# Kernel tuning notes

Measured on AMD Instinct MI355X. Metric: run time of the kernel, lower is better.

Reference implementation:

```python
import jax, jax.numpy as jnp
import numpy as np

N_NODES = 20000
N_EDGES = 320000
F_IN, H1, H2, N_CLS = 128, 512, 256, 40
NEG_SLOPE = 0.2


def _glorot(key, shape):
    lim = float(np.sqrt(6.0 / (shape[0] + shape[-1])))
    return jax.random.uniform(key, shape, jnp.float32, -lim, lim)


def setup_inputs() -> dict:
    key = jax.random.key(0)
    ks = jax.random.split(key, 12)
    x = jax.random.normal(ks[0], (N_NODES, F_IN), jnp.float32)
    edge_index = jax.random.randint(ks[1], (2, N_EDGES), 0, N_NODES, jnp.int64)
    params = {}
    dims = [(F_IN, H1), (H1, H2), (H2, N_CLS)]
    for i, (din, dout) in enumerate(dims, start=1):
        params[f"W{i}"] = _glorot(ks[3 * i - 1], (din, dout))
        params[f"a{i}s"] = _glorot(ks[3 * i], (1, dout))[0]
        params[f"a{i}d"] = _glorot(ks[3 * i + 1], (1, dout))[0]
        params[f"b{i}"] = jnp.zeros((dout,), jnp.float32)
    return {"x": x, "edge_index": edge_index, **params}


def gat_conv(x, src, dst, W, a_src, a_dst, b, num_nodes):
    # PyG GATConv, heads=1: h = xW; e_ij = LeakyReLU(a_src.h_j + a_dst.h_i)
    # alpha = softmax over incoming edges of target i; out_i = sum_j alpha_ij h_j + b
    h = x @ W                                        # [N, Dout]
    alpha_s = h @ a_src                              # [N]
    alpha_d = h @ a_dst                              # [N]
    e = jax.nn.leaky_relu(alpha_s[src] + alpha_d[dst], NEG_SLOPE)  # [E]
    m = jax.ops.segment_max(e, dst, num_segments=num_nodes)        # [N]
    ex = jnp.exp(e - m[dst])
    denom = jax.ops.segment_sum(ex, dst, num_segments=num_nodes)   # [N]
    alpha = ex / denom[dst]
    out = jax.ops.segment_sum(alpha[:, None] * h[src], dst, num_segments=num_nodes)
    return out + b


def reference(x, edge_index, W1, a1s, a1d, b1, W2, a2s, a2d, b2, W3, a3s, a3d, b3):
    n = x.shape[0]
    # PyG GATConv adds self-loops by default
    loops = jnp.arange(n, dtype=edge_index.dtype)
    src = jnp.concatenate([edge_index[0], loops])
    dst = jnp.concatenate([edge_index[1], loops])
    h = jax.nn.relu(gat_conv(x, src, dst, W1, a1s, a1d, b1, n))
    h = jax.nn.relu(gat_conv(h, src, dst, W2, a2s, a2d, b2, n))
    h = gat_conv(h, src, dst, W3, a3s, a3d, b3, n)
    return jax.nn.log_softmax(h, axis=1)
```

## Files before the change

### kernel.cpp

```cpp
#include <hip/hip_runtime.h>
#include <math.h>

#define N_NODES 20000
#define N_EDGESC 320000
#define ET (N_EDGESC + N_NODES)
#define F_IN 128
#define H1 512
#define H2 256
#define N_CLS 40
#define NEG_SLOPE 0.2f

typedef __attribute__((ext_vector_type(8))) short short8;
typedef __attribute__((ext_vector_type(4))) float floatx4;

__device__ __forceinline__ unsigned short f2bf(float x) {
    unsigned u = __float_as_uint(x);
    unsigned r = (u + 0x7fffu + ((u >> 16) & 1u)) >> 16;
    return (unsigned short)r;
}
__device__ __forceinline__ float bflo(unsigned v) { return __uint_as_float(v << 16); }
__device__ __forceinline__ float bfhi(unsigned v) { return __uint_as_float(v & 0xffff0000u); }
__device__ __forceinline__ float leaky(float e) { return (e > 0.f) ? e : e * NEG_SLOPE; }

template <int DIN, bool IN_BF16>
__device__ __forceinline__ void gemv2_body(int node, int lane, const void* __restrict__ in,
                                           const float* __restrict__ wvs,
                                           const float* __restrict__ wvd,
                                           float* __restrict__ als, float* __restrict__ ald) {
    constexpr int C = DIN / 64;
    float ss = 0.f, sd = 0.f;
    if constexpr (IN_BF16) {
        const unsigned short* r = (const unsigned short*)in + (size_t)node * DIN + lane * C;
        float f[C];
        if constexpr (C == 8) {
            uint4 v = *(const uint4*)r;
            f[0] = bflo(v.x); f[1] = bfhi(v.x); f[2] = bflo(v.y); f[3] = bfhi(v.y);
            f[4] = bflo(v.z); f[5] = bfhi(v.z); f[6] = bflo(v.w); f[7] = bfhi(v.w);
        } else {
            uint2 v = *(const uint2*)r;
            f[0] = bflo(v.x); f[1] = bfhi(v.x); f[2] = bflo(v.y); f[3] = bfhi(v.y);
        }
        #pragma unroll
        for (int c = 0; c < C; ++c) {
            ss += f[c] * wvs[lane * C + c];
            sd += f[c] * wvd[lane * C + c];
        }
    } else {
        const float* r = (const float*)in + (size_t)node * DIN + lane * 2;
        float2 v = *(const float2*)r;
        ss = v.x * wvs[lane * 2] + v.y * wvs[lane * 2 + 1];
        sd = v.x * wvd[lane * 2] + v.y * wvd[lane * 2 + 1];
    }
    #pragma unroll
    for (int off = 32; off; off >>= 1) {
        ss += __shfl_xor(ss, off);
        sd += __shfl_xor(sd, off);
    }
    if (lane == 0) { als[node] = ss; ald[node] = sd; }
}

#define NCT (F_IN * H1 + H1 * H2 + H2 * N_CLS)
#define PB_CASTX 2500
#define PB_CASTT ((NCT + 255) / 256)
#define PB_WA 224
#define PB_ZERO ((N_NODES + 255) / 256)

__global__ __launch_bounds__(256) void prep_kernel(
        const float* __restrict__ x, unsigned short* __restrict__ xb,
        const float* __restrict__ W1, unsigned short* __restrict__ w1t,
        const float* __restrict__ a1s, const float* __restrict__ a1d,
        const float* __restrict__ W2, unsigned short* __restrict__ w2t,
        const float* __restrict__ a2s, const float* __restrict__ a2d,
        const float* __restrict__ W3, unsigned short* __restrict__ w3t,
        const float* __restrict__ a3s, const float* __restrict__ a3d,
        float* __restrict__ wab, int* __restrict__ deg) {
    int bid = blockIdx.x, t = threadIdx.x;
    if (bid < PB_CASTX) {
        int i = (bid * 256 + t) * 4;
        float4 v = *(const float4*)(x + i);
        ushort4 o = { f2bf(v.x), f2bf(v.y), f2bf(v.z), f2bf(v.w) };
        *(ushort4*)(xb + i) = o;
    } else if (bid < PB_CASTX + PB_CASTT) {
        int i = (bid - PB_CASTX) * 256 + t;
        if (i < F_IN * H1) {
            int k = i >> 9, n = i & 511;
            w1t[n * F_IN + k] = f2bf(W1[i]);
        } else if (i < F_IN * H1 + H1 * H2) {
            int j = i - F_IN * H1;
            int k = j >> 8, n = j & 255;
            w2t[n * H1 + k] = f2bf(W2[j]);
        } else if (i < NCT) {
            int j = i - (F_IN * H1 + H1 * H2);
            int k = j / N_CLS, n = j - k * N_CLS;
            w3t[n * H2 + k] = f2bf(W3[j]);
        }
    } else if (bid < PB_CASTX + PB_CASTT + PB_WA) {
        int lane = t & 63;
        int row = (bid - PB_CASTX - PB_CASTT) * 4 + (t >> 6);
        const float *W, *vs, *vd;
        float *os, *od;
        int N, k;
        if (row < 128)      { k = row;       W = W1; vs = a1s; vd = a1d; os = wab;        od = wab + 128;  N = H1; }
        else if (row < 640) { k = row - 128; W = W2; vs = a2s; vd = a2d; os = wab + 256;  od = wab + 768;  N = H2; }
        else                { k = row - 640; W = W3; vs = a3s; vd = a3d; os = wab + 1280; od = wab + 1536; N = N_CLS; }
        const float* r = W + (size_t)k * N;
        float ss = 0.f, sd = 0.f;
        for (int n = lane; n < N; n += 64) {
            float v = r[n];
            ss += v * vs[n];
            sd += v * vd[n];
        }
        #pragma unroll
        for (int off = 32; off; off >>= 1) {
            ss += __shfl_xor(ss, off);
            sd += __shfl_xor(sd, off);
        }
        if (lane == 0) { os[k] = ss; od[k] = sd; }
    } else {
        int i = (bid - PB_CASTX - PB_CASTT - PB_WA) * 256 + t;
        if (i < N_NODES) deg[i] = 0;
    }
}

#define CB_CNT ((ET + 255) / 256)

__global__ __launch_bounds__(256) void count_gemv1_kernel(
        const int* __restrict__ ei, int* __restrict__ deg,
        const float* __restrict__ x, const float* __restrict__ wab,
        float* __restrict__ als1, float* __restrict__ ald1) {
    int bid = blockIdx.x, t = threadIdx.x;
    if (bid < CB_CNT) {
        int e = bid * 256 + t;
        if (e < ET) {
            int d = (e < N_EDGESC) ? ei[N_EDGESC + e] : (e - N_EDGESC);
            atomicAdd(&deg[d], 1);
        }
    } else {
        int node = (bid - CB_CNT) * 4 + (t >> 6);
        if (node < N_NODES)
            gemv2_body<F_IN, false>(node, t & 63, x, wab, wab + 128, als1, ald1);
    }
}

__global__ __launch_bounds__(1024) void scan_kernel(const int* __restrict__ deg,
                                                    int* __restrict__ rowptr,
                                                    int* __restrict__ writeptr) {
    __shared__ int sums[1024];
    int t = threadIdx.x;
    const int per = (N_NODES + 1023) / 1024;
    int base = t * per;
    int local = 0;
    for (int i = 0; i < per; ++i) {
        int idx = base + i;
        if (idx < N_NODES) local += deg[idx];
    }
    sums[t] = local;
    __syncthreads();
    for (int off = 1; off < 1024; off <<= 1) {
        int add = (t >= off) ? sums[t - off] : 0;
        __syncthreads();
        sums[t] += add;
        __syncthreads();
    }
    int run = sums[t] - local;
    for (int i = 0; i < per; ++i) {
        int idx = base + i;
        if (idx < N_NODES) {
            rowptr[idx] = run;
            writeptr[idx] = run;
            run += deg[idx];
        }
    }
    if (t == 1023) rowptr[N_NODES] = sums[1023];
}

__global__ void fill_kernel(const int* __restrict__ ei, int* __restrict__ writeptr,
                            int* __restrict__ csr_src) {
    int e = blockIdx.x * blockDim.x + threadIdx.x;
    if (e >= ET) return;
    int s, d;
    if (e < N_EDGESC) { s = ei[e]; d = ei[N_EDGESC + e]; }
    else { s = d = e - N_EDGESC; }
    int pos = atomicAdd(&writeptr[d], 1);
    csr_src[pos] = s;
}

#define LDT 40
#define LSO 66

template <int MT, int NT, bool BIASRELU, bool OUT_BF16, int GDIN, bool GBF16>
__global__ __launch_bounds__(256) void gemm_fused(
        const unsigned short* __restrict__ A, const unsigned short* __restrict__ Bt,
        void* __restrict__ Cp, const float* __restrict__ bias,
        int M, int K, int N, int gemm_blocks,
        const void* __restrict__ gin, const float* __restrict__ wvs,
        const float* __restrict__ wvd, float* __restrict__ als, float* __restrict__ ald) {
    constexpr int MI = MT / 64;
    __shared__ unsigned short As[MT * LDT];
    __shared__ unsigned short Bs[64 * LDT];
    __shared__ unsigned short Ls[64 * LSO];
    int bid = blockIdx.x, t = threadIdx.x;
    int w = t >> 6, lane = t & 63;

    if (bid >= gemm_blocks) {
        if constexpr (GDIN > 0) {
            int node = (bid - gemm_blocks) * 4 + w;
            if (node < N_NODES)
                gemv2_body<GDIN, GBF16>(node, lane, gin, wvs, wvd, als, ald);
        }
        return;
    }

    int quad = lane >> 4, l16 = lane & 15;
    int bm = (bid / NT) * MT, bn = (bid % NT) * 64;

    int ar0 = t >> 2;
    int ak = (t & 3) * 8;

    floatx4 acc[MI][4];
    #pragma unroll
    for (int i = 0; i < MI; ++i)
        #pragma unroll
        for (int j = 0; j < 4; ++j) acc[i][j] = (floatx4){0.f, 0.f, 0.f, 0.f};

    uint4 pa0 = {0,0,0,0}, pa1 = {0,0,0,0}, pb = {0,0,0,0};
    {
        int gm0 = bm + ar0, gn = bn + ar0;
        if (gm0 < M) pa0 = *(const uint4*)(A + (size_t)gm0 * K + ak);
        if constexpr (MI == 2) {
            int gm1 = bm + 64 + ar0;
            if (gm1 < M) pa1 = *(const uint4*)(A + (size_t)gm1 * K + ak);
        }
        if (gn < N) pb = *(const uint4*)(Bt + (size_t)gn * K + ak);
    }

    for (int k0 = 0; k0 < K; k0 += 32) {
        *(uint4*)(&As[ar0 * LDT + ak]) = pa0;
        if constexpr (MI == 2) *(uint4*)(&As[(64 + ar0) * LDT + ak]) = pa1;
        *(uint4*)(&Bs[ar0 * LDT + ak]) = pb;
        __syncthreads();

        int kn = k0 + 32;
        if (kn < K) {
            int gm0 = bm + ar0, gn = bn + ar0;
            pa0 = (gm0 < M) ? *(const uint4*)(A + (size_t)gm0 * K + kn + ak) : (uint4){0,0,0,0};
            if constexpr (MI == 2) {
                int gm1 = bm + 64 + ar0;
                pa1 = (gm1 < M) ? *(const uint4*)(A + (size_t)gm1 * K + kn + ak) : (uint4){0,0,0,0};
            }
            pb = (gn < N) ? *(const uint4*)(Bt + (size_t)gn * K + kn + ak) : (uint4){0,0,0,0};
        }

        short8 a[MI], b[4];
        #pragma unroll
        for (int mi = 0; mi < MI; ++mi)
            a[mi] = *(short8*)(&As[(w * (MT / 4) + mi * 16 + l16) * LDT + quad * 8]);
        #pragma unroll
        for (int ni = 0; ni < 4; ++ni)
            b[ni] = *(short8*)(&Bs[(ni * 16 + l16) * LDT + quad * 8]);
        #pragma unroll
        for (int mi = 0; mi < MI; ++mi)
            #pragma unroll
            for (int ni = 0; ni < 4; ++ni)
                acc[mi][ni] = __builtin_amdgcn_mfma_f32_16x16x32_bf16(a[mi], b[ni], acc[mi][ni], 0, 0, 0);
        __syncthreads();
    }

    if constexpr (OUT_BF16) {
        #pragma unroll
        for (int mi = 0; mi < MI; ++mi) {
            #pragma unroll
            for (int ni = 0; ni < 4; ++ni) {
                int col = bn + ni * 16 + l16;
                #pragma unroll
                for (int r = 0; r < 4; ++r) {
                    float v = acc[mi][ni][r];
                    if constexpr (BIASRELU) v = fmaxf(v + bias[col], 0.f);
                    Ls[(w * 16 + quad * 4 + r) * LSO + ni * 16 + l16] = f2bf(v);
                }
            }
            __syncthreads();
            #pragma unroll
            for (int i = 0; i < 2; ++i) {
                int idx = t + i * 256;
                int lrow = idx >> 3, c8 = (idx & 7) * 8;
                int grow = bm + (lrow >> 4) * (MT / 4) + mi * 16 + (lrow & 15);
                if (grow < M)
                    *(uint4*)((unsigned short*)Cp + (size_t)grow * N + bn + c8) =
                        *(uint4*)(&Ls[lrow * LSO + c8]);
            }
            __syncthreads();
        }
    } else {
        #pragma unroll
        for (int mi = 0; mi < MI; ++mi) {
            #pragma unroll
            for (int r = 0; r < 4; ++r) {
                int row = bm + w * (MT / 4) + mi * 16 + quad * 4 + r;
                if (row >= M) continue;
                #pragma unroll
                for (int ni = 0; ni < 4; ++ni) {
                    int col = bn + ni * 16 + l16;
                    if (col < N) ((float*)Cp)[(size_t)row * N + col] = acc[mi][ni][r];
                }
            }
        }
    }
}

template <int DOUT, bool BIAS, bool RELU, bool LSM, bool IN_BF16, bool OUT_BF16>
__global__ __launch_bounds__(256) void agg_kernel(const void* __restrict__ h,
                                                  const float* __restrict__ as,
                                                  const float* __restrict__ ad,
                                                  const int* __restrict__ rowptr,
                                                  const int* __restrict__ csr_src,
                                                  const float* __restrict__ bias,
                                                  void* __restrict__ outp) {
    constexpr int C = (DOUT + 63) / 64;
    int wave = threadIdx.x >> 6, lane = threadIdx.x & 63;
    int node = blockIdx.x * 4 + wave;
    if (node >= N_NODES) return;
    int beg = rowptr[node], end = rowptr[node + 1];
    float adi = ad[node];

    int k0 = beg + lane;
    bool has0 = k0 < end;
    int sj = has0 ? csr_src[k0] : 0;
    float ej = -INFINITY;
    if (has0) ej = leaky(as[sj] + adi);

    float m = ej;
    for (int k = k0 + 64; k < end; k += 64) m = fmaxf(m, leaky(as[csr_src[k]] + adi));
    #pragma unroll
    for (int off = 32; off; off >>= 1) m = fmaxf(m, __shfl_xor(m, off));

    float den = has0 ? expf(ej - m) : 0.f;
    for (int k = k0 + 64; k < end; k += 64) den += expf(leaky(as[csr_src[k]] + adi) - m);
    #pragma unroll
    for (int off = 32; off; off >>= 1) den += __shfl_xor(den, off);
    float invden = 1.f / den;

    float wgt = has0 ? expf(ej - m) * invden : 0.f;

    float acc[C];
    #pragma unroll
    for (int c = 0; c < C; ++c) acc[c] = 0.f;

    auto fetch = [&](int s, float* f) {
        if constexpr (IN_BF16) {
            const unsigned short* hr = (const unsigned short*)h + (size_t)s * DOUT + lane * C;
            if constexpr (C == 8) {
                uint4 v = *(const uint4*)hr;
                f[0] = bflo(v.x); f[1] = bfhi(v.x); f[2] = bflo(v.y); f[3] = bfhi(v.y);
                f[4] = bflo(v.z); f[5] = bfhi(v.z); f[6] = bflo(v.w); f[7] = bfhi(v.w);
            } else if constexpr (C == 4) {
                uint2 v = *(const uint2*)hr;
                f[0] = bflo(v.x); f[1] = bfhi(v.x); f[2] = bflo(v.y); f[3] = bfhi(v.y);
            } else {
                unsigned v = *(const unsigned*)hr;
                f[0] = bflo(v); f[1] = bfhi(v);
            }
        } else {
            if (lane < DOUT) f[0] = ((const float*)h)[(size_t)s * DOUT + lane];
            else f[0] = 0.f;
        }
    };

    int cnt0 = min(64, end - beg);
    int j = 0;
    for (; j + 7 < cnt0; j += 8) {
        int s[8]; float a[8]; float f[8][C];
        #pragma unroll
        for (int u = 0; u < 8; ++u) { s[u] = __shfl(sj, j + u); a[u] = __shfl(wgt, j + u); }
        #pragma unroll
        for (int u = 0; u < 8; ++u) fetch(s[u], f[u]);
        #pragma unroll
        for (int u = 0; u < 8; ++u)
            #pragma unroll
            for (int c = 0; c < C; ++c) acc[c] += a[u] * f[u][c];
    }
    for (; j < cnt0; ++j) {
        int s0 = __shfl(sj, j);
        float a0 = __shfl(wgt, j);
        float f0[C];
        fetch(s0, f0);
        #pragma unroll
        for (int c = 0; c < C; ++c) acc[c] += a0 * f0[c];
    }
    for (int base = beg + 64; base < end; base += 64) {
        int cnt = min(64, end - base);
        int sx = 0; float wx = 0.f;
        if (lane < cnt) {
            sx = csr_src[base + lane];
            wx = expf(leaky(as[sx] + adi) - m) * invden;
        }
        for (int jj = 0; jj < cnt; ++jj) {
            int s0 = __shfl(sx, jj);
            float a0 = __shfl(wx, jj);
            float f0[C];
            fetch(s0, f0);
            #pragma unroll
            for (int c = 0; c < C; ++c) acc[c] += a0 * f0[c];
        }
    }

    if constexpr (!LSM) {
        #pragma unroll
        for (int c = 0; c < C; ++c) {
            int col = lane * C + c;
            if (DOUT % 64 == 0 || col < DOUT) {
                float v = acc[c];
                if constexpr (BIAS) v += bias[col];
                if constexpr (RELU) v = fmaxf(v, 0.f);
                if constexpr (OUT_BF16)
                    ((unsigned short*)outp)[(size_t)node * DOUT + col] = f2bf(v);
                else
                    ((float*)outp)[(size_t)node * DOUT + col] = v;
            }
        }
    } else {
        float v = (lane < DOUT) ? (acc[0] + bias[lane]) : -INFINITY;
        float mm = v;
        #pragma unroll
        for (int off = 32; off; off >>= 1) mm = fmaxf(mm, __shfl_xor(mm, off));
        float ex = (lane < DOUT) ? expf(v - mm) : 0.f;
        float Z = ex;
        #pragma unroll
        for (int off = 32; off; off >>= 1) Z += __shfl_xor(Z, off);
        if (lane < DOUT) ((float*)outp)[(size_t)node * DOUT + lane] = v - mm - logf(Z);
    }
}


extern "C" void kernel_launch(void* const* d_in, const int* in_sizes, int n_in,
                              void* d_out, int out_size, void* d_ws, size_t ws_size,
                              hipStream_t stream) {
    const float* x   = (const float*)d_in[0];
    const int*   ei  = (const int*)d_in[1];
    const float* W1  = (const float*)d_in[2];
    const float* a1s = (const float*)d_in[3];
    const float* a1d = (const float*)d_in[4];
    const float* b1  = (const float*)d_in[5];
    const float* W2  = (const float*)d_in[6];
    const float* a2s = (const float*)d_in[7];
    const float* a2d = (const float*)d_in[8];
    const float* b2  = (const float*)d_in[9];
    const float* W3  = (const float*)d_in[10];
    const float* a3s = (const float*)d_in[11];
    const float* a3d = (const float*)d_in[12];
    const float* b3  = (const float*)d_in[13];
    float* out = (float*)d_out;

    char* ws = (char*)d_ws;
    size_t off = 0;
    auto alloc = [&](size_t bytes) {
        void* p = ws + off;
        off = (off + bytes + 255) & ~(size_t)255;
        return p;
    };
    int*            deg      = (int*)alloc(N_NODES * 4);
    int*            writeptr = (int*)alloc(N_NODES * 4);
    int*            rowptr   = (int*)alloc((N_NODES + 1) * 4);
    int*            csr_src  = (int*)alloc((size_t)ET * 4);
    float*          alph     = (float*)alloc((size_t)6 * N_NODES * 4);
    float*          wab      = (float*)alloc(1792 * 4);
    unsigned short* xb       = (unsigned short*)alloc((size_t)N_NODES * F_IN * 2);
    unsigned short* w1t      = (unsigned short*)alloc((size_t)H1 * F_IN * 2);
    unsigned short* w2t      = (unsigned short*)alloc((size_t)H2 * H1 * 2);
    unsigned short* w3t      = (unsigned short*)alloc((size_t)N_CLS * H2 * 2);
    unsigned short* zb       = (unsigned short*)alloc((size_t)N_NODES * F_IN * 2);
    unsigned short* y1       = (unsigned short*)alloc((size_t)N_NODES * H1 * 2);
    unsigned short* h2       = (unsigned short*)alloc((size_t)N_NODES * H2 * 2);
    float*          h3       = (float*)alloc((size_t)N_NODES * N_CLS * 4);
    (void)alloc(128 * 1024);

    unsigned short* y2 = y1;

    float* als1 = alph + 0 * N_NODES; float* ald1 = alph + 1 * N_NODES;
    float* als2 = alph + 2 * N_NODES; float* ald2 = alph + 3 * N_NODES;
    float* als3 = alph + 4 * N_NODES; float* ald3 = alph + 5 * N_NODES;

    dim3 blk(256);
    int nodeblocks = (N_NODES + 3) / 4;
    const int mt128 = (N_NODES + 127) / 128;
    const int mt64  = (N_NODES + 63) / 64;

    prep_kernel<<<PB_CASTX + PB_CASTT + PB_WA + PB_ZERO, blk, 0, stream>>>(
        x, xb, W1, w1t, a1s, a1d, W2, w2t, a2s, a2d, W3, w3t, a3s, a3d, wab, deg);
    count_gemv1_kernel<<<CB_CNT + nodeblocks, blk, 0, stream>>>(ei, deg, x, wab, als1, ald1);
    scan_kernel<<<1, 1024, 0, stream>>>(deg, rowptr, writeptr);
    fill_kernel<<<(ET + 255) / 256, blk, 0, stream>>>(ei, writeptr, csr_src);

    agg_kernel<F_IN, false, false, false, true, true><<<nodeblocks, blk, 0, stream>>>(
        xb, als1, ald1, rowptr, csr_src, nullptr, zb);
    gemm_fused<128, 8, true, true, 0, false><<<8 * mt128, blk, 0, stream>>>(
        zb, w1t, y1, b1, N_NODES, F_IN, H1, 8 * mt128,
        nullptr, nullptr, nullptr, nullptr, nullptr);
    gemm_fused<128, 4, false, true, H1, true><<<4 * mt128 + nodeblocks, blk, 0, stream>>>(
        y1, w2t, h2, nullptr, N_NODES, H1, H2, 4 * mt128,
        y1, wab + 256, wab + 768, als2, ald2);
    agg_kernel<H2, true, true, false, true, true><<<nodeblocks, blk, 0, stream>>>(
        h2, als2, ald2, rowptr, csr_src, b2, y2);
    gemm_fused<64, 1, false, false, H2, true><<<mt64 + nodeblocks, blk, 0, stream>>>(
        y2, w3t, h3, nullptr, N_NODES, H2, N_CLS, mt64,
        y2, wab + 1280, wab + 1536, als3, ald3);
    agg_kernel<N_CLS, true, false, true, false, false><<<nodeblocks, blk, 0, stream>>>(
        h3, als3, ald3, rowptr, csr_src, b3, out);
}
```

Baseline: 262.4 us.

## Merge all GAT stages into one persistent cooperative kernel with grid syncs

Replaces the ten separate kernel launches with a single cooperative persistent kernel that loops over virtual blocks per stage and separates stages with grid-wide syncs. The goal is to remove launch overhead and inter-kernel gaps. The GEMM tiles shrink from 128 to 64 rows so one shared-memory layout serves every stage, and the scan now runs on a 256-thread block instead of 1024. In exchange it adds grid-sync costs, caps occupancy at the cooperative grid size, and reduces GEMM tile reuse.

Result: slower. 895.1 us (+241.2%).

```diff
diff --git a/kernel.cpp b/kernel.cpp
--- a/kernel.cpp
+++ b/kernel.cpp
@@ -1,5 +1,8 @@
 #include <hip/hip_runtime.h>
+#include <hip/hip_cooperative_groups.h>
 #include <math.h>
+
+namespace cg = cooperative_groups;
 
 #define N_NODES 20000
 #define N_EDGESC 320000
@@ -9,6 +12,8 @@
 #define H2 256
 #define N_CLS 40
 #define NEG_SLOPE 0.2f
+#define LDT 40
+#define LSO 66
 
 typedef __attribute__((ext_vector_type(8))) short short8;
 typedef __attribute__((ext_vector_type(4))) float floatx4;
@@ -22,11 +27,32 @@
 __device__ __forceinline__ float bfhi(unsigned v) { return __uint_as_float(v & 0xffff0000u); }
 __device__ __forceinline__ float leaky(float e) { return (e > 0.f) ? e : e * NEG_SLOPE; }
 
+struct Params {
+    const float* x; const int* ei;
+    const float *W1, *a1s, *a1d, *b1;
+    const float *W2, *a2s, *a2d, *b2;
+    const float *W3, *a3s, *a3d, *b3;
+    float* out;
+    int *deg, *writeptr, *rowptr, *csr_src;
+    float *alph, *wab;
+    unsigned short *xb, *w1t, *w2t, *w3t, *zb, *y1, *h2;
+    float* h3;
+};
+
+#define NCT (F_IN * H1 + H1 * H2 + H2 * N_CLS)
+#define PB_CASTX 2500
+#define PB_CASTT ((NCT + 255) / 256)
+#define PB_WA 224
+#define PB_ZERO ((N_NODES + 255) / 256)
+#define PB_TOT (PB_CASTX + PB_CASTT + PB_WA + PB_ZERO)
+#define CB_CNT ((ET + 255) / 256)
+#define NODEB ((N_NODES + 3) / 4)
+#define MT64 ((N_NODES + 63) / 64)
+
 template <int DIN, bool IN_BF16>
-__device__ __forceinline__ void gemv2_body(int node, int lane, const void* __restrict__ in,
-                                           const float* __restrict__ wvs,
-                                           const float* __restrict__ wvd,
-                                           float* __restrict__ als, float* __restrict__ ald) {
+__device__ __forceinline__ void gemv2_body(int node, int lane, const void* in,
+                                           const float* wvs, const float* wvd,
+                                           float* als, float* ald) {
     constexpr int C = DIN / 64;
     float ss = 0.f, sd = 0.f;
     if constexpr (IN_BF16) {
@@ -59,40 +85,26 @@
     if (lane == 0) { als[node] = ss; ald[node] = sd; }
 }
 
-#define NCT (F_IN * H1 + H1 * H2 + H2 * N_CLS)
-#define PB_CASTX 2500
-#define PB_CASTT ((NCT + 255) / 256)
-#define PB_WA 224
-#define PB_ZERO ((N_NODES + 255) / 256)
-
-__global__ __launch_bounds__(256) void prep_kernel(
-        const float* __restrict__ x, unsigned short* __restrict__ xb,
-        const float* __restrict__ W1, unsigned short* __restrict__ w1t,
-        const float* __restrict__ a1s, const float* __restrict__ a1d,
-        const float* __restrict__ W2, unsigned short* __restrict__ w2t,
-        const float* __restrict__ a2s, const float* __restrict__ a2d,
-        const float* __restrict__ W3, unsigned short* __restrict__ w3t,
-        const float* __restrict__ a3s, const float* __restrict__ a3d,
-        float* __restrict__ wab, int* __restrict__ deg) {
-    int bid = blockIdx.x, t = threadIdx.x;
+__device__ void prep_vb(int bid, const Params& p) {
+    int t = threadIdx.x;
     if (bid < PB_CASTX) {
         int i = (bid * 256 + t) * 4;
-        float4 v = *(const float4*)(x + i);
+        float4 v = *(const float4*)(p.x + i);
         ushort4 o = { f2bf(v.x), f2bf(v.y), f2bf(v.z), f2bf(v.w) };
-        *(ushort4*)(xb + i) = o;
+        *(ushort4*)(p.xb + i) = o;
     } else if (bid < PB_CASTX + PB_CASTT) {
         int i = (bid - PB_CASTX) * 256 + t;
         if (i < F_IN * H1) {
             int k = i >> 9, n = i & 511;
-            w1t[n * F_IN + k] = f2bf(W1[i]);
+            p.w1t[n * F_IN + k] = f2bf(p.W1[i]);
         } else if (i < F_IN * H1 + H1 * H2) {
             int j = i - F_IN * H1;
             int k = j >> 8, n = j & 255;
-            w2t[n * H1 + k] = f2bf(W2[j]);
+            p.w2t[n * H1 + k] = f2bf(p.W2[j]);
         } else if (i < NCT) {
             int j = i - (F_IN * H1 + H1 * H2);
             int k = j / N_CLS, n = j - k * N_CLS;
-            w3t[n * H2 + k] = f2bf(W3[j]);
+            p.w3t[n * H2 + k] = f2bf(p.W3[j]);
         }
     } else if (bid < PB_CASTX + PB_CASTT + PB_WA) {
         int lane = t & 63;
@@ -100,9 +112,9 @@
         const float *W, *vs, *vd;
         float *os, *od;
         int N, k;
-        if (row < 128)      { k = row;       W = W1; vs = a1s; vd = a1d; os = wab;        od = wab + 128;  N = H1; }
-        else if (row < 640) { k = row - 128; W = W2; vs = a2s; vd = a2d; os = wab + 256;  od = wab + 768;  N = H2; }
-        else                { k = row - 640; W = W3; vs = a3s; vd = a3d; os = wab + 1280; od = wab + 1536; N = N_CLS; }
+        if (row < 128)      { k = row;       W = p.W1; vs = p.a1s; vd = p.a1d; os = p.wab;        od = p.wab + 128;  N = H1; }
+        else if (row < 640) { k = row - 128; W = p.W2; vs = p.a2s; vd = p.a2d; os = p.wab + 256;  od = p.wab + 768;  N = H2; }
+        else                { k = row - 640; W = p.W3; vs = p.a3s; vd = p.a3d; os = p.wab + 1280; od = p.wab + 1536; N = N_CLS; }
         const float* r = W + (size_t)k * N;
         float ss = 0.f, sd = 0.f;
         for (int n = lane; n < N; n += 64) {
@@ -118,45 +130,22 @@
         if (lane == 0) { os[k] = ss; od[k] = sd; }
     } else {
         int i = (bid - PB_CASTX - PB_CASTT - PB_WA) * 256 + t;
-        if (i < N_NODES) deg[i] = 0;
-    }
-}
-
-#define CB_CNT ((ET + 255) / 256)
-
-__global__ __launch_bounds__(256) void count_gemv1_kernel(
-        const int* __restrict__ ei, int* __restrict__ deg,
-        const float* __restrict__ x, const float* __restrict__ wab,
-        float* __restrict__ als1, float* __restrict__ ald1) {
-    int bid = blockIdx.x, t = threadIdx.x;
-    if (bid < CB_CNT) {
-        int e = bid * 256 + t;
-        if (e < ET) {
-            int d = (e < N_EDGESC) ? ei[N_EDGESC + e] : (e - N_EDGESC);
-            atomicAdd(&deg[d], 1);
-        }
-    } else {
-        int node = (bid - CB_CNT) * 4 + (t >> 6);
-        if (node < N_NODES)
-            gemv2_body<F_IN, false>(node, t & 63, x, wab, wab + 128, als1, ald1);
-    }
-}
-
-__global__ __launch_bounds__(1024) void scan_kernel(const int* __restrict__ deg,
-                                                    int* __restrict__ rowptr,
-                                                    int* __restrict__ writeptr) {
-    __shared__ int sums[1024];
+        if (i < N_NODES) p.deg[i] = 0;
+    }
+}
+
+__device__ void scan256(const Params& p, int* sums) {
     int t = threadIdx.x;
-    const int per = (N_NODES + 1023) / 1024;
+    const int per = (N_NODES + 255) / 256;
     int base = t * per;
     int local = 0;
     for (int i = 0; i < per; ++i) {
         int idx = base + i;
-        if (idx < N_NODES) local += deg[idx];
+        if (idx < N_NODES) local += p.deg[idx];
     }
     sums[t] = local;
     __syncthreads();
-    for (int off = 1; off < 1024; off <<= 1) {
+    for (int off = 1; off < 256; off <<= 1) {
         int add = (t >= off) ? sums[t - off] : 0;
         __syncthreads();
         sums[t] += add;
@@ -166,160 +155,109 @@
     for (int i = 0; i < per; ++i) {
         int idx = base + i;
         if (idx < N_NODES) {
-            rowptr[idx] = run;
-            writeptr[idx] = run;
-            run += deg[idx];
-        }
-    }
-    if (t == 1023) rowptr[N_NODES] = sums[1023];
-}
-
-__global__ void fill_kernel(const int* __restrict__ ei, int* __restrict__ writeptr,
-                            int* __restrict__ csr_src) {
-    int e = blockIdx.x * blockDim.x + threadIdx.x;
+            p.rowptr[idx] = run;
+            p.writeptr[idx] = run;
+            run += p.deg[idx];
+        }
+    }
+    if (t == 255) p.rowptr[N_NODES] = sums[255];
+}
+
+__device__ void fill_vb(int bid, const Params& p) {
+    int e = bid * 256 + threadIdx.x;
     if (e >= ET) return;
     int s, d;
-    if (e < N_EDGESC) { s = ei[e]; d = ei[N_EDGESC + e]; }
+    if (e < N_EDGESC) { s = p.ei[e]; d = p.ei[N_EDGESC + e]; }
     else { s = d = e - N_EDGESC; }
-    int pos = atomicAdd(&writeptr[d], 1);
-    csr_src[pos] = s;
-}
-
-#define LDT 40
-#define LSO 66
-
-template <int MT, int NT, bool BIASRELU, bool OUT_BF16, int GDIN, bool GBF16>
-__global__ __launch_bounds__(256) void gemm_fused(
-        const unsigned short* __restrict__ A, const unsigned short* __restrict__ Bt,
-        void* __restrict__ Cp, const float* __restrict__ bias,
-        int M, int K, int N, int gemm_blocks,
-        const void* __restrict__ gin, const float* __restrict__ wvs,
-        const float* __restrict__ wvd, float* __restrict__ als, float* __restrict__ ald) {
-    constexpr int MI = MT / 64;
-    __shared__ unsigned short As[MT * LDT];
-    __shared__ unsigned short Bs[64 * LDT];
-    __shared__ unsigned short Ls[64 * LSO];
-    int bid = blockIdx.x, t = threadIdx.x;
+    int pos = atomicAdd(&p.writeptr[d], 1);
+    p.csr_src[pos] = s;
+}
+
+template <int NT, bool BIASRELU, bool OUT_BF16>
+__device__ void gemm64_vb(int vb, const unsigned short* __restrict__ A,
+                          const unsigned short* __restrict__ Bt,
+                          void* __restrict__ Cp, const float* __restrict__ bias,
+                          int M, int K, int N,
+                          unsigned short* As, unsigned short* Bs, unsigned short* Ls) {
+    int t = threadIdx.x;
     int w = t >> 6, lane = t & 63;
-
-    if (bid >= gemm_blocks) {
-        if constexpr (GDIN > 0) {
-            int node = (bid - gemm_blocks) * 4 + w;
-            if (node < N_NODES)
-                gemv2_body<GDIN, GBF16>(node, lane, gin, wvs, wvd, als, ald);
-        }
-        return;
-    }
-
     int quad = lane >> 4, l16 = lane & 15;
-    int bm = (bid / NT) * MT, bn = (bid % NT) * 64;
-
-    int ar0 = t >> 2;
-    int ak = (t & 3) * 8;
-
-    floatx4 acc[MI][4];
+    int bm = (vb / NT) * 64, bn = (vb % NT) * 64;
+    int ar = t >> 2, ak = (t & 3) * 8;
+    int gm = bm + ar, gn = bn + ar;
+
+    floatx4 acc[4];
     #pragma unroll
-    for (int i = 0; i < MI; ++i)
-        #pragma unroll
-        for (int j = 0; j < 4; ++j) acc[i][j] = (floatx4){0.f, 0.f, 0.f, 0.f};
-
-    uint4 pa0 = {0,0,0,0}, pa1 = {0,0,0,0}, pb = {0,0,0,0};
-    {
-        int gm0 = bm + ar0, gn = bn + ar0;
-        if (gm0 < M) pa0 = *(const uint4*)(A + (size_t)gm0 * K + ak);
-        if constexpr (MI == 2) {
-            int gm1 = bm + 64 + ar0;
-            if (gm1 < M) pa1 = *(const uint4*)(A + (size_t)gm1 * K + ak);
-        }
-        if (gn < N) pb = *(const uint4*)(Bt + (size_t)gn * K + ak);
-    }
+    for (int j = 0; j < 4; ++j) acc[j] = (floatx4){0.f, 0.f, 0.f, 0.f};
+
+    uint4 pa = {0,0,0,0}, pb = {0,0,0,0};
+    if (gm < M) pa = *(const uint4*)(A + (size_t)gm * K + ak);
+    if (gn < N) pb = *(const uint4*)(Bt + (size_t)gn * K + ak);
 
     for (int k0 = 0; k0 < K; k0 += 32) {
-        *(uint4*)(&As[ar0 * LDT + ak]) = pa0;
-        if constexpr (MI == 2) *(uint4*)(&As[(64 + ar0) * LDT + ak]) = pa1;
-        *(uint4*)(&Bs[ar0 * LDT + ak]) = pb;
+        *(uint4*)(&As[ar * LDT + ak]) = pa;
+        *(uint4*)(&Bs[ar * LDT + ak]) = pb;
         __syncthreads();
 
         int kn = k0 + 32;
         if (kn < K) {
-            int gm0 = bm + ar0, gn = bn + ar0;
-            pa0 = (gm0 < M) ? *(const uint4*)(A + (size_t)gm0 * K + kn + ak) : (uint4){0,0,0,0};
-            if constexpr (MI == 2) {
-                int gm1 = bm + 64 + ar0;
-                pa1 = (gm1 < M) ? *(const uint4*)(A + (size_t)gm1 * K + kn + ak) : (uint4){0,0,0,0};
-            }
+            pa = (gm < M) ? *(const uint4*)(A + (size_t)gm * K + kn + ak) : (uint4){0,0,0,0};
             pb = (gn < N) ? *(const uint4*)(Bt + (size_t)gn * K + kn + ak) : (uint4){0,0,0,0};
         }
 
-        short8 a[MI], b[4];
-        #pragma unroll
-        for (int mi = 0; mi < MI; ++mi)
-            a[mi] = *(short8*)(&As[(w * (MT / 4) + mi * 16 + l16) * LDT + quad * 8]);
+        short8 a = *(short8*)(&As[(w * 16 + l16) * LDT + quad * 8]);
+        short8 b[4];
         #pragma unroll
         for (int ni = 0; ni < 4; ++ni)
             b[ni] = *(short8*)(&Bs[(ni * 16 + l16) * LDT + quad * 8]);
         #pragma unroll
-        for (int mi = 0; mi < MI; ++mi)
+        for (int ni = 0; ni < 4; ++ni)
+            acc[ni] = __builtin_amdgcn_mfma_f32_16x16x32_bf16(a, b[ni], acc[ni], 0, 0, 0);
+        __syncthreads();
+    }
+
+    if constexpr (OUT_BF16) {
+        #pragma unroll
+        for (int ni = 0; ni < 4; ++ni) {
+            int col = bn + ni * 16 + l16;
             #pragma unroll
-            for (int ni = 0; ni < 4; ++ni)
-                acc[mi][ni] = __builtin_amdgcn_mfma_f32_16x16x32_bf16(a[mi], b[ni], acc[mi][ni], 0, 0, 0);
-        __syncthreads();
-    }
-
-    if constexpr (OUT_BF16) {
-        #pragma unroll
-        for (int mi = 0; mi < MI; ++mi) {
+            for (int r = 0; r < 4; ++r) {
+                float v = acc[ni][r];
+                if constexpr (BIASRELU) v = fmaxf(v + bias[col], 0.f);
+                Ls[(w * 16 + quad * 4 + r) * LSO + ni * 16 + l16] = f2bf(v);
+            }
+        }
+        __syncthreads();
+        #pragma unroll
+        for (int i = 0; i < 2; ++i) {
+            int idx = t + i * 256;
+            int lrow = idx >> 3, c8 = (idx & 7) * 8;
+            int grow = bm + lrow;
+            if (grow < M)
+                *(uint4*)((unsigned short*)Cp + (size_t)grow * N + bn + c8) =
+                    *(uint4*)(&Ls[lrow * LSO + c8]);
+        }
+        __syncthreads();
+    } else {
+        #pragma unroll
+        for (int r = 0; r < 4; ++r) {
+            int row = bm + w * 16 + quad * 4 + r;
+            if (row >= M) continue;
             #pragma unroll
             for (int ni = 0; ni < 4; ++ni) {
                 int col = bn + ni * 16 + l16;
-                #pragma unroll
-                for (int r = 0; r < 4; ++r) {
-                    float v = acc[mi][ni][r];
-                    if constexpr (BIASRELU) v = fmaxf(v + bias[col], 0.f);
-                    Ls[(w * 16 + quad * 4 + r) * LSO + ni * 16 + l16] = f2bf(v);
-                }
+                if (col < N) ((float*)Cp)[(size_t)row * N + col] = acc[ni][r];
             }
-            __syncthreads();
-            #pragma unroll
-            for (int i = 0; i < 2; ++i) {
-                int idx = t + i * 256;
-                int lrow = idx >> 3, c8 = (idx & 7) * 8;
-                int grow = bm + (lrow >> 4) * (MT / 4) + mi * 16 + (lrow & 15);
-                if (grow < M)
-                    *(uint4*)((unsigned short*)Cp + (size_t)grow * N + bn + c8) =
-                        *(uint4*)(&Ls[lrow * LSO + c8]);
-            }
-            __syncthreads();
-        }
-    } else {
-        #pragma unroll
-        for (int mi = 0; mi < MI; ++mi) {
-            #pragma unroll
-            for (int r = 0; r < 4; ++r) {
-                int row = bm + w * (MT / 4) + mi * 16 + quad * 4 + r;
-                if (row >= M) continue;
-                #pragma unroll
-                for (int ni = 0; ni < 4; ++ni) {
-                    int col = bn + ni * 16 + l16;
-                    if (col < N) ((float*)Cp)[(size_t)row * N + col] = acc[mi][ni][r];
-                }
-            }
         }
     }
 }
 
 template <int DOUT, bool BIAS, bool RELU, bool LSM, bool IN_BF16, bool OUT_BF16>
-__global__ __launch_bounds__(256) void agg_kernel(const void* __restrict__ h,
-                                                  const float* __restrict__ as,
-                                                  const float* __restrict__ ad,
-                                                  const int* __restrict__ rowptr,
-                                                  const int* __restrict__ csr_src,
-                                                  const float* __restrict__ bias,
-                                                  void* __restrict__ outp) {
+__device__ void agg_node(int node, int lane, const void* __restrict__ h,
+                         const float* __restrict__ as, const float* __restrict__ ad,
+                         const int* __restrict__ rowptr, const int* __restrict__ csr_src,
+                         const float* __restrict__ bias, void* __restrict__ outp) {
     constexpr int C = (DOUT + 63) / 64;
-    int wave = threadIdx.x >> 6, lane = threadIdx.x & 63;
-    int node = blockIdx.x * 4 + wave;
-    if (node >= N_NODES) return;
     int beg = rowptr[node], end = rowptr[node + 1];
     float adi = ad[node];
 
@@ -431,26 +369,87 @@
     }
 }
 
+__global__ __launch_bounds__(256, 4) void mega(Params p) {
+    cg::grid_group g = cg::this_grid();
+    const int nb = gridDim.x, bx = blockIdx.x;
+    const int t = threadIdx.x, w = t >> 6, lane = t & 63;
+    __shared__ unsigned short As[64 * LDT];
+    __shared__ unsigned short Bs[64 * LDT];
+    __shared__ unsigned short Ls[64 * LSO];
+
+    float* als1 = p.alph + 0 * N_NODES; float* ald1 = p.alph + 1 * N_NODES;
+    float* als2 = p.alph + 2 * N_NODES; float* ald2 = p.alph + 3 * N_NODES;
+    float* als3 = p.alph + 4 * N_NODES; float* ald3 = p.alph + 5 * N_NODES;
+
+    for (int vb = bx; vb < PB_TOT; vb += nb) prep_vb(vb, p);
+    g.sync();
+    for (int vb = bx; vb < CB_CNT + NODEB; vb += nb) {
+        if (vb < CB_CNT) {
+            int e = vb * 256 + t;
+            if (e < ET) {
+                int d = (e < N_EDGESC) ? p.ei[N_EDGESC + e] : (e - N_EDGESC);
+                atomicAdd(&p.deg[d], 1);
+            }
+        } else {
+            int node = (vb - CB_CNT) * 4 + w;
+            if (node < N_NODES)
+                gemv2_body<F_IN, false>(node, lane, p.x, p.wab, p.wab + 128, als1, ald1);
+        }
+    }
+    g.sync();
+    if (bx == 0) scan256(p, (int*)As);
+    g.sync();
+    for (int vb = bx; vb < CB_CNT; vb += nb) fill_vb(vb, p);
+    g.sync();
+    for (int vb = bx; vb < NODEB; vb += nb) {
+        int node = vb * 4 + w;
+        if (node < N_NODES)
+            agg_node<F_IN, false, false, false, true, true>(
+                node, lane, p.xb, als1, ald1, p.rowptr, p.csr_src, nullptr, p.zb);
+    }
+    g.sync();
+    for (int vb = bx; vb < MT64 * 8; vb += nb)
+        gemm64_vb<8, true, true>(vb, p.zb, p.w1t, p.y1, p.b1, N_NODES, F_IN, H1, As, Bs, Ls);
+    g.sync();
+    for (int vb = bx; vb < MT64 * 4 + NODEB; vb += nb) {
+        if (vb < MT64 * 4)
+            gemm64_vb<4, false, true>(vb, p.y1, p.w2t, p.h2, nullptr, N_NODES, H1, H2, As, Bs, Ls);
+        else {
+            int node = (vb - MT64 * 4) * 4 + w;
+            if (node < N_NODES)
+                gemv2_body<H1, true>(node, lane, p.y1, p.wab + 256, p.wab + 768, als2, ald2);
+        }
+    }
+    g.sync();
+    for (int vb = bx; vb < NODEB; vb += nb) {
+        int node = vb * 4 + w;
+        if (node < N_NODES)
+            agg_node<H2, true, true, false, true, true>(
+                node, lane, p.h2, als2, ald2, p.rowptr, p.csr_src, p.b2, p.y1);
+    }
+    g.sync();
+    for (int vb = bx; vb < MT64 + NODEB; vb += nb) {
+        if (vb < MT64)
+            gemm64_vb<1, false, false>(vb, p.y1, p.w3t, p.h3, nullptr, N_NODES, H2, N_CLS, As, Bs, Ls);
+        else {
+            int node = (vb - MT64) * 4 + w;
+            if (node < N_NODES)
+                gemv2_body<H2, true>(node, lane, p.y1, p.wab + 1280, p.wab + 1536, als3, ald3);
+        }
+    }
+    g.sync();
+    for (int vb = bx; vb < NODEB; vb += nb) {
+        int node = vb * 4 + w;
+        if (node < N_NODES)
+            agg_node<N_CLS, true, false, true, false, false>(
+                node, lane, p.h3, als3, ald3, p.rowptr, p.csr_src, p.b3, p.out);
+    }
+}
+
 
 extern "C" void kernel_launch(void* const* d_in, const int* in_sizes, int n_in,
                               void* d_out, int out_size, void* d_ws, size_t ws_size,
                               hipStream_t stream) {
-    const float* x   = (const float*)d_in[0];
-    const int*   ei  = (const int*)d_in[1];
-    const float* W1  = (const float*)d_in[2];
-    const float* a1s = (const float*)d_in[3];
-    const float* a1d = (const float*)d_in[4];
-    const float* b1  = (const float*)d_in[5];
-    const float* W2  = (const float*)d_in[6];
-    const float* a2s = (const float*)d_in[7];
-    const float* a2d = (const float*)d_in[8];
-    const float* b2  = (const float*)d_in[9];
-    const float* W3  = (const float*)d_in[10];
-    const float* a3s = (const float*)d_in[11];
-    const float* a3d = (const float*)d_in[12];
-    const float* b3  = (const float*)d_in[13];
-    float* out = (float*)d_out;
-
     char* ws = (char*)d_ws;
     size_t off = 0;
     auto alloc = [&](size_t bytes) {
@@ -458,52 +457,39 @@
         off = (off + bytes + 255) & ~(size_t)255;
         return p;
     };
-    int*            deg      = (int*)alloc(N_NODES * 4);
-    int*            writeptr = (int*)alloc(N_NODES * 4);
-    int*            rowptr   = (int*)alloc((N_NODES + 1) * 4);
-    int*            csr_src  = (int*)alloc((size_t)ET * 4);
-    float*          alph     = (float*)alloc((size_t)6 * N_NODES * 4);
-    float*          wab      = (float*)alloc(1792 * 4);
-    unsigned short* xb       = (unsigned short*)alloc((size_t)N_NODES * F_IN * 2);
-    unsigned short* w1t      = (unsigned short*)alloc((size_t)H1 * F_IN * 2);
-    unsigned short* w2t      = (unsigned short*)alloc((size_t)H2 * H1 * 2);
-    unsigned short* w3t      = (unsigned short*)alloc((size_t)N_CLS * H2 * 2);
-    unsigned short* zb       = (unsigned short*)alloc((size_t)N_NODES * F_IN * 2);
-    unsigned short* y1       = (unsigned short*)alloc((size_t)N_NODES * H1 * 2);
-    unsigned short* h2       = (unsigned short*)alloc((size_t)N_NODES * H2 * 2);
-    float*          h3       = (float*)alloc((size_t)N_NODES * N_CLS * 4);
+    Params p;
+    p.x   = (const float*)d_in[0];
+    p.ei  = (const int*)d_in[1];
+    p.W1  = (const float*)d_in[2];  p.a1s = (const float*)d_in[3];
+    p.a1d = (const float*)d_in[4];  p.b1  = (const float*)d_in[5];
+    p.W2  = (const float*)d_in[6];  p.a2s = (const float*)d_in[7];
+    p.a2d = (const float*)d_in[8];  p.b2  = (const float*)d_in[9];
+    p.W3  = (const float*)d_in[10]; p.a3s = (const float*)d_in[11];
+    p.a3d = (const float*)d_in[12]; p.b3  = (const float*)d_in[13];
+    p.out = (float*)d_out;
+
+    p.deg      = (int*)alloc(N_NODES * 4);
+    p.writeptr = (int*)alloc(N_NODES * 4);
+    p.rowptr   = (int*)alloc((N_NODES + 1) * 4);
+    p.csr_src  = (int*)alloc((size_t)ET * 4);
+    p.alph     = (float*)alloc((size_t)6 * N_NODES * 4);
+    p.wab      = (float*)alloc(1792 * 4);
+    p.xb       = (unsigned short*)alloc((size_t)N_NODES * F_IN * 2);
+    p.w1t      = (unsigned short*)alloc((size_t)H1 * F_IN * 2);
+    p.w2t      = (unsigned short*)alloc((size_t)H2 * H1 * 2);
+    p.w3t      = (unsigned short*)alloc((size_t)N_CLS * H2 * 2);
+    p.zb       = (unsigned short*)alloc((size_t)N_NODES * F_IN * 2);
+    p.y1       = (unsigned short*)alloc((size_t)N_NODES * H1 * 2);
+    p.h2       = (unsigned short*)alloc((size_t)N_NODES * H2 * 2);
+    p.h3       = (float*)alloc((size_t)N_NODES * N_CLS * 4);
     (void)alloc(128 * 1024);
 
-    unsigned short* y2 = y1;
-
-    float* als1 = alph + 0 * N_NODES; float* ald1 = alph + 1 * N_NODES;
-    float* als2 = alph + 2 * N_NODES; float* ald2 = alph + 3 * N_NODES;
-    float* als3 = alph + 4 * N_NODES; float* ald3 = alph + 5 * N_NODES;
-
-    dim3 blk(256);
-    int nodeblocks = (N_NODES + 3) / 4;
-    const int mt128 = (N_NODES + 127) / 128;
-    const int mt64  = (N_NODES + 63) / 64;
-
-    prep_kernel<<<PB_CASTX + PB_CASTT + PB_WA + PB_ZERO, blk, 0, stream>>>(
-        x, xb, W1, w1t, a1s, a1d, W2, w2t, a2s, a2d, W3, w3t, a3s, a3d, wab, deg);
-    count_gemv1_kernel<<<CB_CNT + nodeblocks, blk, 0, stream>>>(ei, deg, x, wab, als1, ald1);
-    scan_kernel<<<1, 1024, 0, stream>>>(deg, rowptr, writeptr);
-    fill_kernel<<<(ET + 255) / 256, blk, 0, stream>>>(ei, writeptr, csr_src);
-
-    agg_kernel<F_IN, false, false, false, true, true><<<nodeblocks, blk, 0, stream>>>(
-        xb, als1, ald1, rowptr, csr_src, nullptr, zb);
-    gemm_fused<128, 8, true, true, 0, false><<<8 * mt128, blk, 0, stream>>>(
-        zb, w1t, y1, b1, N_NODES, F_IN, H1, 8 * mt128,
-        nullptr, nullptr, nullptr, nullptr, nullptr);
-    gemm_fused<128, 4, false, true, H1, true><<<4 * mt128 + nodeblocks, blk, 0, stream>>>(
-        y1, w2t, h2, nullptr, N_NODES, H1, H2, 4 * mt128,
-        y1, wab + 256, wab + 768, als2, ald2);
-    agg_kernel<H2, true, true, false, true, true><<<nodeblocks, blk, 0, stream>>>(
-        h2, als2, ald2, rowptr, csr_src, b2, y2);
-    gemm_fused<64, 1, false, false, H2, true><<<mt64 + nodeblocks, blk, 0, stream>>>(
-        y2, w3t, h3, nullptr, N_NODES, H2, N_CLS, mt64,
-        y2, wab + 1280, wab + 1536, als3, ald3);
-    agg_kernel<N_CLS, true, false, true, false, false><<<nodeblocks, blk, 0, stream>>>(
-        h3, als3, ald3, rowptr, csr_src, b3, out);
-}
+    int maxb = 0;
+    hipOccupancyMaxActiveBlocksPerMultiprocessor(&maxb, mega, 256, 0);
+    if (maxb < 1) maxb = 1;
+    long long grid = (long long)maxb * 256;
+    if (grid > 2048) grid = 2048;
+
+    void* args[] = { &p };
+    hipLaunchCooperativeKernel(mega, dim3((unsigned)grid), dim3(256), args, 0, stream);
+}
```

## Fuse attention-logit dot products into GEMM and aggregation epilogues

Applied to the files above, without the earlier changes.

The separate gemv blocks that computed per-node attention logits (reading y1 and y2 again) are removed. Layer-2 logits are now accumulated in the layer-1 GEMM epilogue through shuffle reductions and atomicAdd into buffers that are zeroed in the prep kernel. Layer-3 logits are computed in the layer-2 aggregation epilogue with a wave reduction. This saves re-reading large activation matrices, at the cost of atomics and nondeterministic fp32 summation order. The logits now come from fp32 values before bf16 rounding, so they differ slightly from before.

Measured after the change: 267.4 us. About the same (+1.9%).

```diff
diff --git a/kernel.cpp b/kernel.cpp
--- a/kernel.cpp
+++ b/kernel.cpp
@@ -63,7 +63,7 @@
 #define PB_CASTX 2500
 #define PB_CASTT ((NCT + 255) / 256)
 #define PB_WA 224
-#define PB_ZERO ((N_NODES + 255) / 256)
+#define PB_ZERO ((3 * N_NODES + 255) / 256)
 
 __global__ __launch_bounds__(256) void prep_kernel(
         const float* __restrict__ x, unsigned short* __restrict__ xb,
@@ -73,7 +73,7 @@
         const float* __restrict__ a2s, const float* __restrict__ a2d,
         const float* __restrict__ W3, unsigned short* __restrict__ w3t,
         const float* __restrict__ a3s, const float* __restrict__ a3d,
-        float* __restrict__ wab, int* __restrict__ deg) {
+        float* __restrict__ wab, int* __restrict__ deg, float* __restrict__ alph) {
     int bid = blockIdx.x, t = threadIdx.x;
     if (bid < PB_CASTX) {
         int i = (bid * 256 + t) * 4;
@@ -119,6 +119,7 @@
     } else {
         int i = (bid - PB_CASTX - PB_CASTT - PB_WA) * 256 + t;
         if (i < N_NODES) deg[i] = 0;
+        else if (i < 3 * N_NODES) alph[2 * N_NODES + (i - N_NODES)] = 0.f;
     }
 }
 
@@ -188,29 +189,19 @@
 #define LDT 40
 #define LSO 66
 
-template <int MT, int NT, bool BIASRELU, bool OUT_BF16, int GDIN, bool GBF16>
+template <int MT, int NT, bool BIASRELU, bool OUT_BF16, bool ALPHA>
 __global__ __launch_bounds__(256) void gemm_fused(
         const unsigned short* __restrict__ A, const unsigned short* __restrict__ Bt,
         void* __restrict__ Cp, const float* __restrict__ bias,
-        int M, int K, int N, int gemm_blocks,
-        const void* __restrict__ gin, const float* __restrict__ wvs,
-        const float* __restrict__ wvd, float* __restrict__ als, float* __restrict__ ald) {
+        int M, int K, int N,
+        const float* __restrict__ av_s, const float* __restrict__ av_d,
+        float* __restrict__ o_s, float* __restrict__ o_d) {
     constexpr int MI = MT / 64;
     __shared__ unsigned short As[MT * LDT];
     __shared__ unsigned short Bs[64 * LDT];
     __shared__ unsigned short Ls[64 * LSO];
     int bid = blockIdx.x, t = threadIdx.x;
     int w = t >> 6, lane = t & 63;
-
-    if (bid >= gemm_blocks) {
-        if constexpr (GDIN > 0) {
-            int node = (bid - gemm_blocks) * 4 + w;
-            if (node < N_NODES)
-                gemv2_body<GDIN, GBF16>(node, lane, gin, wvs, wvd, als, ald);
-        }
-        return;
-    }
-
     int quad = lane >> 4, l16 = lane & 15;
     int bm = (bid / NT) * MT, bn = (bid % NT) * 64;
 
@@ -269,14 +260,38 @@
     if constexpr (OUT_BF16) {
         #pragma unroll
         for (int mi = 0; mi < MI; ++mi) {
+            float ps[4] = {0.f, 0.f, 0.f, 0.f}, pd[4] = {0.f, 0.f, 0.f, 0.f};
             #pragma unroll
             for (int ni = 0; ni < 4; ++ni) {
                 int col = bn + ni * 16 + l16;
+                float avs = 0.f, avd = 0.f;
+                if constexpr (ALPHA) { avs = av_s[col]; avd = av_d[col]; }
                 #pragma unroll
                 for (int r = 0; r < 4; ++r) {
                     float v = acc[mi][ni][r];
                     if constexpr (BIASRELU) v = fmaxf(v + bias[col], 0.f);
+                    if constexpr (ALPHA) { ps[r] += v * avs; pd[r] += v * avd; }
                     Ls[(w * 16 + quad * 4 + r) * LSO + ni * 16 + l16] = f2bf(v);
+                }
+            }
+            if constexpr (ALPHA) {
+                #pragma unroll
+                for (int r = 0; r < 4; ++r) {
+                    #pragma unroll
+                    for (int msk = 1; msk <= 8; msk <<= 1) {
+                        ps[r] += __shfl_xor(ps[r], msk);
+                        pd[r] += __shfl_xor(pd[r], msk);
+                    }
+                }
+                if (l16 == 0) {
+                    #pragma unroll
+                    for (int r = 0; r < 4; ++r) {
+                        int row = bm + w * (MT / 4) + mi * 16 + quad * 4 + r;
+                        if (row < M) {
+                            atomicAdd(&o_s[row], ps[r]);
+                            atomicAdd(&o_d[row], pd[r]);
+                        }
+                    }
                 }
             }
             __syncthreads();
@@ -308,14 +323,18 @@
     }
 }
 
-template <int DOUT, bool BIAS, bool RELU, bool LSM, bool IN_BF16, bool OUT_BF16>
+template <int DOUT, bool BIAS, bool RELU, bool LSM, bool IN_BF16, bool OUT_BF16, bool ALPHA3>
 __global__ __launch_bounds__(256) void agg_kernel(const void* __restrict__ h,
                                                   const float* __restrict__ as,
                                                   const float* __restrict__ ad,
                                                   const int* __restrict__ rowptr,
                                                   const int* __restrict__ csr_src,
                                                   const float* __restrict__ bias,
-                                                  void* __restrict__ outp) {
+                                                  void* __restrict__ outp,
+                                                  const float* __restrict__ wv3s,
+                                                  const float* __restrict__ wv3d,
+                                                  float* __restrict__ o3s,
+                                                  float* __restrict__ o3d) {
     constexpr int C = (DOUT + 63) / 64;
     int wave = threadIdx.x >> 6, lane = threadIdx.x & 63;
     int node = blockIdx.x * 4 + wave;
@@ -405,6 +424,7 @@
     }
 
     if constexpr (!LSM) {
+        float ps = 0.f, pd = 0.f;
         #pragma unroll
         for (int c = 0; c < C; ++c) {
             int col = lane * C + c;
@@ -412,11 +432,20 @@
                 float v = acc[c];
                 if constexpr (BIAS) v += bias[col];
                 if constexpr (RELU) v = fmaxf(v, 0.f);
+                if constexpr (ALPHA3) { ps += v * wv3s[col]; pd += v * wv3d[col]; }
                 if constexpr (OUT_BF16)
                     ((unsigned short*)outp)[(size_t)node * DOUT + col] = f2bf(v);
                 else
                     ((float*)outp)[(size_t)node * DOUT + col] = v;
             }
+        }
+        if constexpr (ALPHA3) {
+            #pragma unroll
+            for (int off = 32; off; off >>= 1) {
+                ps += __shfl_xor(ps, off);
+                pd += __shfl_xor(pd, off);
+            }
+            if (lane == 0) { o3s[node] = ps; o3d[node] = pd; }
         }
     } else {
         float v = (lane < DOUT) ? (acc[0] + bias[lane]) : -INFINITY;
@@ -486,24 +515,21 @@
     const int mt64  = (N_NODES + 63) / 64;
 
     prep_kernel<<<PB_CASTX + PB_CASTT + PB_WA + PB_ZERO, blk, 0, stream>>>(
-        x, xb, W1, w1t, a1s, a1d, W2, w2t, a2s, a2d, W3, w3t, a3s, a3d, wab, deg);
+        x, xb, W1, w1t, a1s, a1d, W2, w2t, a2s, a2d, W3, w3t, a3s, a3d, wab, deg, alph);
     count_gemv1_kernel<<<CB_CNT + nodeblocks, blk, 0, stream>>>(ei, deg, x, wab, als1, ald1);
     scan_kernel<<<1, 1024, 0, stream>>>(deg, rowptr, writeptr);
     fill_kernel<<<(ET + 255) / 256, blk, 0, stream>>>(ei, writeptr, csr_src);
 
-    agg_kernel<F_IN, false, false, false, true, true><<<nodeblocks, blk, 0, stream>>>(
-        xb, als1, ald1, rowptr, csr_src, nullptr, zb);
-    gemm_fused<128, 8, true, true, 0, false><<<8 * mt128, blk, 0, stream>>>(
-        zb, w1t, y1, b1, N_NODES, F_IN, H1, 8 * mt128,
-        nullptr, nullptr, nullptr, nullptr, nullptr);
-    gemm_fused<128, 4, false, true, H1, true><<<4 * mt128 + nodeblocks, blk, 0, stream>>>(
-        y1, w2t, h2, nullptr, N_NODES, H1, H2, 4 * mt128,
-        y1, wab + 256, wab + 768, als2, ald2);
-    agg_kernel<H2, true, true, false, true, true><<<nodeblocks, blk, 0, stream>>>(
-        h2, als2, ald2, rowptr, csr_src, b2, y2);
-    gemm_fused<64, 1, false, false, H2, true><<<mt64 + nodeblocks, blk, 0, stream>>>(
-        y2, w3t, h3, nullptr, N_NODES, H2, N_CLS, mt64,
-        y2, wab + 1280, wab + 1536, als3, ald3);
-    agg_kernel<N_CLS, true, false, true, false, false><<<nodeblocks, blk, 0, stream>>>(
-        h3, als3, ald3, rowptr, csr_src, b3, out);
-}
+    agg_kernel<F_IN, false, false, false, true, true, false><<<nodeblocks, blk, 0, stream>>>(
+        xb, als1, ald1, rowptr, csr_src, nullptr, zb, nullptr, nullptr, nullptr, nullptr);
+    gemm_fused<128, 8, true, true, true><<<8 * mt128, blk, 0, stream>>>(
+        zb, w1t, y1, b1, N_NODES, F_IN, H1, wab + 256, wab + 768, als2, ald2);
+    gemm_fused<128, 4, false, true, false><<<4 * mt128, blk, 0, stream>>>(
+        y1, w2t, h2, nullptr, N_NODES, H1, H2, nullptr, nullptr, nullptr, nullptr);
+    agg_kernel<H2, true, true, false, true, true, true><<<nodeblocks, blk, 0, stream>>>(
+        h2, als2, ald2, rowptr, csr_src, b2, y2, wab + 1280, wab + 1536, als3, ald3);
+    gemm_fused<64, 1, false, false, false><<<mt64, blk, 0, stream>>>(
+        y2, w3t, h3, nullptr, N_NODES, H2, N_CLS, nullptr, nullptr, nullptr, nullptr);
+    agg_kernel<N_CLS, true, false, true, false, false, false><<<nodeblocks, blk, 0, stream>>>(
+        h3, als3, ald3, rowptr, csr_src, b3, out, nullptr, nullptr, nullptr, nullptr);
+}
```
